# Optimization experiments

Hardware: AMD Instinct MI355X
Metric: run time of the kernel (lower is better)

The kernel has to match this reference:

```python
import jax, jax.numpy as jnp
import numpy as np

B, D, H, O, E, TOP_K = 1024, 1024, 2048, 1024, 8, 2


def setup_inputs() -> dict:
    key = jax.random.key(0)
    ks = jax.random.split(key, 8)
    s = 0.02
    return {
        "x":  jax.random.normal(ks[0], (B, D), dtype=jnp.float32),
        "Wr": jax.random.normal(ks[1], (D, E), dtype=jnp.float32) * s,
        "br": jnp.zeros((E,), dtype=jnp.float32),
        "W1": jax.random.normal(ks[2], (E, D, H), dtype=jnp.float32) * s,
        "b1": jnp.zeros((E, H), dtype=jnp.float32),
        "W2": jax.random.normal(ks[3], (E, H, H), dtype=jnp.float32) * s,
        "b2": jnp.zeros((E, H), dtype=jnp.float32),
        "W3": jax.random.normal(ks[4], (E, H, O), dtype=jnp.float32) * s,
        "b3": jnp.zeros((E, O), dtype=jnp.float32),
    }


def reference(x, Wr, br, W1, b1, W2, b2, W3, b3):
    # --- router: softmax -> top-k -> renormalize selected weights ---
    logits = x @ Wr + br                      # [B, E]
    probs = jax.nn.softmax(logits, axis=-1)
    w, ids = jax.lax.top_k(probs, TOP_K)      # [B, K], [B, K]
    w = w / (jnp.sum(w, axis=-1, keepdims=True) + 1e-6)

    # --- expert MLPs (depth=2: in->h, relu, h->h, relu, h->out) ---
    h = jax.nn.relu(jnp.einsum('bd,edh->beh', x, W1) + b1)   # [B, E, H]
    h = jax.nn.relu(jnp.einsum('beh,ehg->beg', h, W2) + b2)  # [B, E, H]
    y_e = jnp.einsum('beg,ego->beo', h, W3) + b3             # [B, E, O]

    # --- weighted scatter-combine: comb[b,e] = sum_k w[b,k] * [ids[b,k]==e] ---
    comb = jnp.sum(jax.nn.one_hot(ids, E, dtype=x.dtype) * w[..., None], axis=1)  # [B, E]
    out = jnp.einsum('beo,be->bo', y_e, comb)                # [B, O]
    return out
```

## Files before the change

### kernel.cpp

```cpp
#include <hip/hip_runtime.h>
#include <hip/hip_bf16.h>

#define BT 1024
#define DD 1024
#define HH 2048
#define OO 1024
#define EE 8
#define RMAX 3072

typedef __bf16 bf16x8 __attribute__((ext_vector_type(8)));
typedef float  f32x4  __attribute__((ext_vector_type(4)));

__device__ __forceinline__ void cp16(void* l, const void* g) {
    __builtin_amdgcn_global_load_lds(
        (const __attribute__((address_space(1))) void*)g,
        (__attribute__((address_space(3))) void*)l, 16, 0, 0);
}

#define VMW(n)  asm volatile("s_waitcnt vmcnt(" #n ")" ::: "memory")
#define LGKM(n) asm volatile("s_waitcnt lgkmcnt(" #n ")" ::: "memory")
#define SCHED0  __builtin_amdgcn_sched_barrier(0)
#define BAR()   __builtin_amdgcn_s_barrier()


__global__ __launch_bounds__(256) void router_kernel(
    const float* __restrict__ x, const float* __restrict__ Wr, const float* __restrict__ br,
    int* __restrict__ counts, int* __restrict__ elist,
    int* __restrict__ tok_e, int* __restrict__ tok_p, float* __restrict__ tok_w)
{
    int b = blockIdx.x;
    int tid = threadIdx.x;
    float acc[EE];
#pragma unroll
    for (int e = 0; e < EE; ++e) acc[e] = 0.f;
    const float* xr = x + (size_t)b * DD;
    for (int d = tid; d < DD; d += 256) {
        float xv = xr[d];
#pragma unroll
        for (int e = 0; e < EE; ++e) acc[e] += xv * Wr[d * EE + e];
    }
    __shared__ float red[4][EE];
    int lane = tid & 63, wv = tid >> 6;
#pragma unroll
    for (int e = 0; e < EE; ++e) {
        float v = acc[e];
#pragma unroll
        for (int o = 32; o > 0; o >>= 1) v += __shfl_down(v, o, 64);
        if (lane == 0) red[wv][e] = v;
    }
    __syncthreads();
    if (tid == 0) {
        float lg[EE];
#pragma unroll
        for (int e = 0; e < EE; ++e) lg[e] = red[0][e] + red[1][e] + red[2][e] + red[3][e] + br[e];
        float mx = lg[0];
#pragma unroll
        for (int e = 1; e < EE; ++e) mx = fmaxf(mx, lg[e]);
        float s = 0.f, p[EE];
#pragma unroll
        for (int e = 0; e < EE; ++e) { p[e] = expf(lg[e] - mx); s += p[e]; }
        float inv = 1.f / s;
#pragma unroll
        for (int e = 0; e < EE; ++e) p[e] *= inv;
        int i0 = 0; float b0 = p[0];
#pragma unroll
        for (int e = 1; e < EE; ++e) if (p[e] > b0) { b0 = p[e]; i0 = e; }
        int i1 = -1; float b1v = -1.f;
#pragma unroll
        for (int e = 0; e < EE; ++e) if (e != i0 && p[e] > b1v) { b1v = p[e]; i1 = e; }
        float s2 = b0 + b1v + 1e-6f;
        float w0 = b0 / s2, w1 = b1v / s2;
        int p0 = atomicAdd(&counts[i0], 1);
        int p1 = atomicAdd(&counts[i1], 1);
        elist[i0 * 1024 + p0] = b;
        elist[i1 * 1024 + p1] = b;
        tok_e[2 * b] = i0; tok_e[2 * b + 1] = i1;
        tok_p[2 * b] = p0; tok_p[2 * b + 1] = p1;
        tok_w[2 * b] = w0; tok_w[2 * b + 1] = w1;
    }
}

__global__ void offsets_kernel(const int* __restrict__ counts, int* __restrict__ off)
{
    if (threadIdx.x == 0 && blockIdx.x == 0) {
        int a = 0;
        for (int e = 0; e < EE; ++e) {
            off[e] = a;
            a += ((counts[e] + 127) >> 7) << 7;
        }
        off[EE] = a;
    }
}

__global__ __launch_bounds__(256) void gather_kernel(
    const float* __restrict__ x, const int* __restrict__ counts, const int* __restrict__ off,
    const int* __restrict__ elist, __bf16* __restrict__ Xg)
{
    int e = blockIdx.y;
    int chunk = blockIdx.x >> 2;
    int rg = blockIdx.x & 3;
    int cnt = counts[e];
    if (chunk * 128 >= cnt) return;
    int base = off[e] + chunk * 128 + rg * 32;
    int tid = threadIdx.x;
    for (int it = 0; it < 32; ++it) {
        int slot = chunk * 128 + rg * 32 + it;
        __bf16 v[4];
        if (slot < cnt) {
            int tok = elist[e * 1024 + slot];
            const float4 f = *(const float4*)(x + (size_t)tok * DD + tid * 4);
            v[0] = (__bf16)f.x; v[1] = (__bf16)f.y; v[2] = (__bf16)f.z; v[3] = (__bf16)f.w;
        } else {
            v[0] = v[1] = v[2] = v[3] = (__bf16)0.f;
        }
        *(uint2*)(Xg + (size_t)(base + it) * DD + tid * 4) = *(uint2*)v;
    }
}

template <int K, int N>
__global__ __launch_bounds__(256) void wprep(const float* __restrict__ W, __bf16* __restrict__ Wb)
{
    constexpr int NSL = N / 512;
    int ks = blockIdx.x, e = blockIdx.y;
    int t = threadIdx.x;
    const float* Wp = W + (size_t)e * K * N + (size_t)ks * 64 * N;
    __shared__ __bf16 T[512 * 72];

    for (int s = 0; s < NSL; ++s) {
#pragma unroll
        for (int i = 0; i < 4; ++i) {
            int tau = i * 256 + t;
            int nti = tau & 127;
            int kt  = tau >> 7;
            float4 f[8];
#pragma unroll
            for (int rr = 0; rr < 8; ++rr)
                f[rr] = *(const float4*)(Wp + (size_t)(kt * 8 + rr) * N + s * 512 + nti * 4);
#pragma unroll
            for (int j = 0; j < 4; ++j) {
                __bf16 t8[8];
#pragma unroll
                for (int rr = 0; rr < 8; ++rr) t8[rr] = (__bf16)((&f[rr].x)[j]);
                *(uint4*)(&T[(nti * 4 + j) * 72 + kt * 8]) = *(uint4*)t8;
            }
        }
        __syncthreads();
#pragma unroll
        for (int i = 0; i < 16; ++i) {
            int idx = i * 256 + t;
            int ntg = idx >> 9;
            int rem = idx & 511;
            int n = rem >> 3, c = rem & 7;
            uint4 v = *(const uint4*)(&T[(ntg * 64 + n) * 72 + (c ^ (n & 7)) * 8]);
            size_t dst = ((((size_t)e * (N / 64) + (s * 8 + ntg)) * (K / 64) + ks) << 12) + (size_t)rem * 8;
            *(uint4*)(&Wb[dst]) = v;
        }
        __syncthreads();
    }
}

template <int K, int N, bool RELU, bool OUT_BF16>
__global__ __launch_bounds__(256, 2) void gemm_fused(
    const __bf16* __restrict__ A, const __bf16* __restrict__ Wb,
    const float* __restrict__ bias, void* __restrict__ OutV,
    const int* __restrict__ counts, const int* __restrict__ off)
{
    constexpr int NSTEPS = K / 64;

    int e  = blockIdx.x & 7;
    int nt = blockIdx.x >> 3;
    int mt = blockIdx.y;
    int cnt = counts[e];
    if (mt * 128 >= cnt) return;
    int row0 = off[e] + mt * 128;

    const __bf16* Ab = A + (size_t)row0 * K;
    const __bf16* Bp = Wb + ((size_t)e * (N / 64) + nt) * (size_t)(K / 64) * 4096;

    __shared__ __bf16 As[3 * 8192];
    __shared__ __bf16 Bs[3 * 4096];

    int tid = threadIdx.x;
    int wave = tid >> 6, lane = tid & 63;
    int m = lane & 15, q = lane >> 4;
    int wm = (wave >> 1) * 64, wn = (wave & 1) * 32;

    int rdma = wave * 8 + (lane >> 3);
    int kxe  = ((lane & 7) ^ (lane >> 3)) * 8;

    f32x4 acc[4][2] = {};

    auto issue = [&](int t) {
        unsigned ab = (unsigned)(t % 3) * 8192;
        unsigned bb = (unsigned)(t % 3) * 4096;
#pragma unroll
        for (int i = 0; i < 4; ++i)
            cp16(&As[ab + i * 2048 + wave * 512 + lane * 8],
                 Ab + (size_t)(i * 32 + rdma) * K + t * 64 + kxe);
#pragma unroll
        for (int r = 0; r < 2; ++r)
            cp16(&Bs[bb + r * 2048 + wave * 512 + lane * 8],
                 Bp + (size_t)t * 4096 + r * 2048 + wave * 512 + lane * 8);
    };

    issue(0);
    issue(1);

    for (int t = 0; t < NSTEPS; ++t) {
        if (t == NSTEPS - 1) { VMW(0); } else { VMW(6); }
        SCHED0;
        BAR();
        SCHED0;
        if (t + 2 < NSTEPS) issue(t + 2);

        unsigned aR = (unsigned)(t % 3) * 8192;
        unsigned bR = (unsigned)(t % 3) * 4096;
        bf16x8 af0[4], bf0[2], af1[4], bf1[2];
#pragma unroll
        for (int i = 0; i < 4; ++i)
            af0[i] = *(bf16x8*)(&As[aR + (wm + i * 16 + m) * 64 + ((q) ^ (m & 7)) * 8]);
#pragma unroll
        for (int j = 0; j < 2; ++j)
            bf0[j] = *(bf16x8*)(&Bs[bR + (wn + j * 16 + m) * 64 + ((q) ^ (m & 7)) * 8]);
        SCHED0;
#pragma unroll
        for (int i = 0; i < 4; ++i)
            af1[i] = *(bf16x8*)(&As[aR + (wm + i * 16 + m) * 64 + ((4 + q) ^ (m & 7)) * 8]);
#pragma unroll
        for (int j = 0; j < 2; ++j)
            bf1[j] = *(bf16x8*)(&Bs[bR + (wn + j * 16 + m) * 64 + ((4 + q) ^ (m & 7)) * 8]);
        LGKM(6); SCHED0;
        __builtin_amdgcn_s_setprio(1);
#pragma unroll
        for (int i = 0; i < 4; ++i)
#pragma unroll
            for (int j = 0; j < 2; ++j)
                acc[i][j] = __builtin_amdgcn_mfma_f32_16x16x32_bf16(af0[i], bf0[j], acc[i][j], 0, 0, 0);
        LGKM(0); SCHED0;
#pragma unroll
        for (int i = 0; i < 4; ++i)
#pragma unroll
            for (int j = 0; j < 2; ++j)
                acc[i][j] = __builtin_amdgcn_mfma_f32_16x16x32_bf16(af1[i], bf1[j], acc[i][j], 0, 0, 0);
        __builtin_amdgcn_s_setprio(0);
    }

    const float* bp = bias + (size_t)e * N;
    int colbase = nt * 64 + wn;
#pragma unroll
    for (int j = 0; j < 2; ++j) {
        int col = colbase + j * 16 + m;
        float bv = bp[col];
#pragma unroll
        for (int i = 0; i < 4; ++i) {
            int rbase = row0 + wm + i * 16 + q * 4;
#pragma unroll
            for (int r = 0; r < 4; ++r) {
                float v = acc[i][j][r] + bv;
                if constexpr (RELU) v = fmaxf(v, 0.f);
                if constexpr (OUT_BF16)
                    ((__bf16*)OutV)[(size_t)(rbase + r) * N + col] = (__bf16)v;
                else
                    ((float*)OutV)[(size_t)(rbase + r) * N + col] = v;
            }
        }
    }
}

__global__ __launch_bounds__(256) void combine_kernel(
    const float* __restrict__ Y, const int* __restrict__ off,
    const int* __restrict__ tok_e, const int* __restrict__ tok_p,
    const float* __restrict__ tok_w, float* __restrict__ out)
{
    int b = blockIdx.x, t = threadIdx.x;
    int e0 = tok_e[2 * b], e1 = tok_e[2 * b + 1];
    int r0 = off[e0] + tok_p[2 * b];
    int r1 = off[e1] + tok_p[2 * b + 1];
    float w0 = tok_w[2 * b], w1 = tok_w[2 * b + 1];
    int col = t * 4;
    f32x4 s0 = *(const f32x4*)(Y + (size_t)r0 * OO + col);
    f32x4 s1 = *(const f32x4*)(Y + (size_t)r1 * OO + col);
    f32x4 o = s0 * w0 + s1 * w1;
    *(f32x4*)(out + (size_t)b * OO + col) = o;
}

extern "C" void kernel_launch(void* const* d_in, const int* in_sizes, int n_in,
                              void* d_out, int out_size, void* d_ws, size_t ws_size,
                              hipStream_t stream)
{
    (void)in_sizes; (void)n_in; (void)out_size; (void)ws_size;
    const float* x  = (const float*)d_in[0];
    const float* Wr = (const float*)d_in[1];
    const float* br = (const float*)d_in[2];
    const float* W1 = (const float*)d_in[3];
    const float* b1 = (const float*)d_in[4];
    const float* W2 = (const float*)d_in[5];
    const float* b2 = (const float*)d_in[6];
    const float* W3 = (const float*)d_in[7];
    const float* b3 = (const float*)d_in[8];
    float* out = (float*)d_out;

    char* ws = (char*)d_ws;
    int*    counts = (int*)(ws + 0);
    int*    off    = (int*)(ws + 256);
    int*    tok_e  = (int*)(ws + 1024);
    int*    tok_p  = (int*)(ws + 9216);
    float*  tok_w  = (float*)(ws + 17408);
    int*    elist  = (int*)(ws + 25600);
    __bf16* Xg     = (__bf16*)(ws + 65536);
    __bf16* H1     = (__bf16*)(ws + 6356992);
    __bf16* H2     = (__bf16*)(ws + 18939904);
    float*  Y      = (float*)(ws + 31522816);
    __bf16* Wb1    = (__bf16*)(ws + 44105728);
    __bf16* Wb2    = (__bf16*)(ws + 77660160);
    __bf16* Wb3    = (__bf16*)(ws + 144769024);

    hipMemsetAsync(counts, 0, 256, stream);
    router_kernel<<<1024, 256, 0, stream>>>(x, Wr, br, counts, elist, tok_e, tok_p, tok_w);
    offsets_kernel<<<1, 64, 0, stream>>>(counts, off);
    gather_kernel<<<dim3(32, 8), 256, 0, stream>>>(x, counts, off, elist, Xg);

    wprep<1024, 2048><<<dim3(16, 8), 256, 0, stream>>>(W1, Wb1);
    wprep<2048, 2048><<<dim3(32, 8), 256, 0, stream>>>(W2, Wb2);
    wprep<2048, 1024><<<dim3(32, 8), 256, 0, stream>>>(W3, Wb3);

    gemm_fused<1024, 2048, true,  true ><<<dim3(256, 8), 256, 0, stream>>>(Xg, Wb1, b1, (void*)H1, counts, off);
    gemm_fused<2048, 2048, true,  true ><<<dim3(256, 8), 256, 0, stream>>>(H1, Wb2, b2, (void*)H2, counts, off);
    gemm_fused<2048, 1024, false, false><<<dim3(128, 8), 256, 0, stream>>>(H2, Wb3, b3, (void*)Y,  counts, off);

    combine_kernel<<<1024, 256, 0, stream>>>(Y, off, tok_e, tok_p, tok_w, out);
}
```

Measured before the change: 496.4 us.

## Switch MoE GEMM to BK=32 four-stage pipeline with matching weight-prep layout

Halves the K-step of the grouped expert GEMM from 64 to 32, uses four LDS buffers with three tiles in flight, and raises the occupancy hint to 3 blocks per CU. The weight-prep kernel is rewritten to emit the new 32-wide tile layout with a different swizzle, staging a full 32xN slab in LDS with 512 threads. The intent is more in-flight memory loads and higher occupancy to hide latency, at the cost of twice as many barriers per K and less MFMA work per sync. The new wprep uses 64-128KB of LDS per block and reads LDS with strided scalar loads that may cause bank conflicts.

```diff
diff --git a/kernel.cpp b/kernel.cpp
--- a/kernel.cpp
+++ b/kernel.cpp
@@ -118,54 +118,48 @@
 }
 
 template <int K, int N>
-__global__ __launch_bounds__(256) void wprep(const float* __restrict__ W, __bf16* __restrict__ Wb)
-{
-    constexpr int NSL = N / 512;
-    int ks = blockIdx.x, e = blockIdx.y;
+__global__ __launch_bounds__(512, 1) void wprep(const float* __restrict__ W, __bf16* __restrict__ Wb)
+{
+    int kb = blockIdx.x, e = blockIdx.y;
     int t = threadIdx.x;
-    const float* Wp = W + (size_t)e * K * N + (size_t)ks * 64 * N;
-    __shared__ __bf16 T[512 * 72];
-
-    for (int s = 0; s < NSL; ++s) {
-#pragma unroll
-        for (int i = 0; i < 4; ++i) {
-            int tau = i * 256 + t;
-            int nti = tau & 127;
-            int kt  = tau >> 7;
-            float4 f[8];
-#pragma unroll
-            for (int rr = 0; rr < 8; ++rr)
-                f[rr] = *(const float4*)(Wp + (size_t)(kt * 8 + rr) * N + s * 512 + nti * 4);
-#pragma unroll
-            for (int j = 0; j < 4; ++j) {
-                __bf16 t8[8];
-#pragma unroll
-                for (int rr = 0; rr < 8; ++rr) t8[rr] = (__bf16)((&f[rr].x)[j]);
-                *(uint4*)(&T[(nti * 4 + j) * 72 + kt * 8]) = *(uint4*)t8;
-            }
-        }
-        __syncthreads();
-#pragma unroll
-        for (int i = 0; i < 16; ++i) {
-            int idx = i * 256 + t;
-            int ntg = idx >> 9;
-            int rem = idx & 511;
-            int n = rem >> 3, c = rem & 7;
-            uint4 v = *(const uint4*)(&T[(ntg * 64 + n) * 72 + (c ^ (n & 7)) * 8]);
-            size_t dst = ((((size_t)e * (N / 64) + (s * 8 + ntg)) * (K / 64) + ks) << 12) + (size_t)rem * 8;
-            *(uint4*)(&Wb[dst]) = v;
-        }
-        __syncthreads();
+    const float* Wp = W + (size_t)e * K * N + (size_t)kb * 32 * N;
+    __shared__ __bf16 T[32 * N];
+
+#pragma unroll
+    for (int j = 0; j < N / 64; ++j) {
+        int g = j * 512 + t;
+        int row = g >> (N == 2048 ? 9 : 8);
+        int n4 = g & (N / 4 - 1);
+        float4 f = *(const float4*)(Wp + (size_t)row * N + n4 * 4);
+        __bf16 v[4] = { (__bf16)f.x, (__bf16)f.y, (__bf16)f.z, (__bf16)f.w };
+        *(uint2*)(&T[row * N + n4 * 4]) = *(uint2*)v;
+    }
+    __syncthreads();
+
+    __bf16* Wbp = Wb + (((size_t)e * (N / 64)) * (K / 32) + kb) * 2048;
+#pragma unroll
+    for (int rnd = 0; rnd < (N / 64) * 256 / 512; ++rnd) {
+        int c = rnd * 512 + t;
+        int nt = c >> 8;
+        int cid = c & 255;
+        int n = cid >> 2, slot = cid & 3;
+        int q = slot ^ ((n >> 1) & 3);
+        __bf16 v[8];
+#pragma unroll
+        for (int kk = 0; kk < 8; ++kk)
+            v[kk] = T[(q * 8 + kk) * N + nt * 64 + n];
+        __bf16* dst = Wbp + (size_t)nt * (K / 32) * 2048 + n * 32 + slot * 8;
+        *(uint4*)dst = *(uint4*)v;
     }
 }
 
 template <int K, int N, bool RELU, bool OUT_BF16>
-__global__ __launch_bounds__(256, 2) void gemm_fused(
+__global__ __launch_bounds__(256, 3) void gemm_fused(
     const __bf16* __restrict__ A, const __bf16* __restrict__ Wb,
     const float* __restrict__ bias, void* __restrict__ OutV,
     const int* __restrict__ counts, const int* __restrict__ off)
 {
-    constexpr int NSTEPS = K / 64;
+    constexpr int NSTEPS = K / 32;
 
     int e  = blockIdx.x & 7;
     int nt = blockIdx.x >> 3;
@@ -175,73 +169,62 @@
     int row0 = off[e] + mt * 128;
 
     const __bf16* Ab = A + (size_t)row0 * K;
-    const __bf16* Bp = Wb + ((size_t)e * (N / 64) + nt) * (size_t)(K / 64) * 4096;
-
-    __shared__ __bf16 As[3 * 8192];
-    __shared__ __bf16 Bs[3 * 4096];
+    const __bf16* Bp = Wb + ((size_t)e * (N / 64) + nt) * (size_t)(K / 32) * 2048;
+
+    __shared__ __bf16 As[4 * 4096];
+    __shared__ __bf16 Bs[4 * 2048];
 
     int tid = threadIdx.x;
     int wave = tid >> 6, lane = tid & 63;
     int m = lane & 15, q = lane >> 4;
     int wm = (wave >> 1) * 64, wn = (wave & 1) * 32;
 
-    int rdma = wave * 8 + (lane >> 3);
-    int kxe  = ((lane & 7) ^ (lane >> 3)) * 8;
+    int adr = lane >> 2;
+    int asrc = ((lane & 3) ^ ((lane >> 3) & 3)) * 8;
 
     f32x4 acc[4][2] = {};
 
     auto issue = [&](int t) {
-        unsigned ab = (unsigned)(t % 3) * 8192;
-        unsigned bb = (unsigned)(t % 3) * 4096;
-#pragma unroll
-        for (int i = 0; i < 4; ++i)
-            cp16(&As[ab + i * 2048 + wave * 512 + lane * 8],
-                 Ab + (size_t)(i * 32 + rdma) * K + t * 64 + kxe);
-#pragma unroll
-        for (int r = 0; r < 2; ++r)
-            cp16(&Bs[bb + r * 2048 + wave * 512 + lane * 8],
-                 Bp + (size_t)t * 4096 + r * 2048 + wave * 512 + lane * 8);
+        unsigned ab = (unsigned)(t & 3) * 4096;
+        unsigned bb = (unsigned)(t & 3) * 2048;
+        int s0 = wave * 32, s1 = wave * 32 + 16;
+        cp16(&As[ab + wave * 1024 + lane * 8],
+             Ab + (size_t)(s0 + adr) * K + t * 32 + asrc);
+        cp16(&As[ab + wave * 1024 + 512 + lane * 8],
+             Ab + (size_t)(s1 + adr) * K + t * 32 + asrc);
+        cp16(&Bs[bb + wave * 512 + lane * 8],
+             Bp + (size_t)t * 2048 + wave * 512 + lane * 8);
     };
 
-    issue(0);
-    issue(1);
+    issue(0); issue(1); issue(2);
 
     for (int t = 0; t < NSTEPS; ++t) {
-        if (t == NSTEPS - 1) { VMW(0); } else { VMW(6); }
+        if (t + 3 < NSTEPS) { VMW(6); } else { VMW(0); }
         SCHED0;
         BAR();
         SCHED0;
-        if (t + 2 < NSTEPS) issue(t + 2);
-
-        unsigned aR = (unsigned)(t % 3) * 8192;
-        unsigned bR = (unsigned)(t % 3) * 4096;
-        bf16x8 af0[4], bf0[2], af1[4], bf1[2];
+        if (t + 3 < NSTEPS) issue(t + 3);
+
+        unsigned aR = (unsigned)(t & 3) * 4096;
+        unsigned bR = (unsigned)(t & 3) * 2048;
+        bf16x8 af[4], bfr[2];
+#pragma unroll
+        for (int i = 0; i < 4; ++i) {
+            int row = wm + i * 16 + m;
+            af[i] = *(bf16x8*)(&As[aR + row * 32 + (q ^ ((row >> 1) & 3)) * 8]);
+        }
+#pragma unroll
+        for (int j = 0; j < 2; ++j) {
+            int n = wn + j * 16 + m;
+            bfr[j] = *(bf16x8*)(&Bs[bR + n * 32 + (q ^ ((n >> 1) & 3)) * 8]);
+        }
+        LGKM(0); SCHED0;
+        __builtin_amdgcn_s_setprio(1);
 #pragma unroll
         for (int i = 0; i < 4; ++i)
-            af0[i] = *(bf16x8*)(&As[aR + (wm + i * 16 + m) * 64 + ((q) ^ (m & 7)) * 8]);
-#pragma unroll
-        for (int j = 0; j < 2; ++j)
-            bf0[j] = *(bf16x8*)(&Bs[bR + (wn + j * 16 + m) * 64 + ((q) ^ (m & 7)) * 8]);
-        SCHED0;
-#pragma unroll
-        for (int i = 0; i < 4; ++i)
-            af1[i] = *(bf16x8*)(&As[aR + (wm + i * 16 + m) * 64 + ((4 + q) ^ (m & 7)) * 8]);
-#pragma unroll
-        for (int j = 0; j < 2; ++j)
-            bf1[j] = *(bf16x8*)(&Bs[bR + (wn + j * 16 + m) * 64 + ((4 + q) ^ (m & 7)) * 8]);
-        LGKM(6); SCHED0;
-        __builtin_amdgcn_s_setprio(1);
-#pragma unroll
-        for (int i = 0; i < 4; ++i)
 #pragma unroll
             for (int j = 0; j < 2; ++j)
-                acc[i][j] = __builtin_amdgcn_mfma_f32_16x16x32_bf16(af0[i], bf0[j], acc[i][j], 0, 0, 0);
-        LGKM(0); SCHED0;
-#pragma unroll
-        for (int i = 0; i < 4; ++i)
-#pragma unroll
-            for (int j = 0; j < 2; ++j)
-                acc[i][j] = __builtin_amdgcn_mfma_f32_16x16x32_bf16(af1[i], bf1[j], acc[i][j], 0, 0, 0);
+                acc[i][j] = __builtin_amdgcn_mfma_f32_16x16x32_bf16(af[i], bfr[j], acc[i][j], 0, 0, 0);
         __builtin_amdgcn_s_setprio(0);
     }
 
@@ -320,9 +303,9 @@
     offsets_kernel<<<1, 64, 0, stream>>>(counts, off);
     gather_kernel<<<dim3(32, 8), 256, 0, stream>>>(x, counts, off, elist, Xg);
 
-    wprep<1024, 2048><<<dim3(16, 8), 256, 0, stream>>>(W1, Wb1);
-    wprep<2048, 2048><<<dim3(32, 8), 256, 0, stream>>>(W2, Wb2);
-    wprep<2048, 1024><<<dim3(32, 8), 256, 0, stream>>>(W3, Wb3);
+    wprep<1024, 2048><<<dim3(32, 8), 512, 0, stream>>>(W1, Wb1);
+    wprep<2048, 2048><<<dim3(64, 8), 512, 0, stream>>>(W2, Wb2);
+    wprep<2048, 1024><<<dim3(64, 8), 512, 0, stream>>>(W3, Wb3);
 
     gemm_fused<1024, 2048, true,  true ><<<dim3(256, 8), 256, 0, stream>>>(Xg, Wb1, b1, (void*)H1, counts, off);
     gemm_fused<2048, 2048, true,  true ><<<dim3(256, 8), 256, 0, stream>>>(H1, Wb2, b2, (void*)H2, counts, off);
```

New measurement: 495.9 us. No clear change (-0.1%).
